# Performance work log

Measured on AMD Instinct MI355X. Metric: run time of the kernel, lower is better.

The kernel has to match this reference:

```python
import jax, jax.numpy as jnp
import numpy as np

N_NODES = 50000


def setup_inputs() -> dict:
    key = jax.random.key(0)
    k1, k2, k3, k4 = jax.random.split(key, 4)
    x = jax.random.normal(k1, (N_NODES, 128), dtype=jnp.float32)
    edge_index = jax.random.randint(k2, (2, 1600000), 0, N_NODES, dtype=jnp.int64)
    W1 = jax.random.normal(k3, (128, 256), dtype=jnp.float32) * (1.0 / np.sqrt(128))
    b1 = jnp.zeros((256,), dtype=jnp.float32)
    W2 = jax.random.normal(k4, (256, 1), dtype=jnp.float32) * (1.0 / np.sqrt(256))
    b2 = jnp.zeros((1,), dtype=jnp.float32)
    return {"x": x, "edge_index": edge_index, "W1": W1, "b1": b1, "W2": W2, "b2": b2}


def _gcn_conv(x, src, dst, norm, W, b, n_nodes):
    # PyG GCNConv: h = X W; out_i = sum_j norm_ij * h_j (+ self loop) + b
    h = x @ W                               # [N, F_out]
    msg = h[src] * norm[:, None]            # [E', F_out] gather + scale
    out = jax.ops.segment_sum(msg, dst, num_segments=n_nodes)  # scatter-add
    return out + b


def reference(x, edge_index, W1, b1, W2, b2):
    n = x.shape[0]
    loop = jnp.arange(n, dtype=edge_index.dtype)
    src = jnp.concatenate([edge_index[0], loop])   # add self loops
    dst = jnp.concatenate([edge_index[1], loop])
    # symmetric degree normalization on A + I
    deg = jax.ops.segment_sum(jnp.ones_like(dst, dtype=x.dtype), dst, num_segments=n)
    dis = jnp.where(deg > 0, jax.lax.rsqrt(deg), 0.0)
    norm = dis[src] * dis[dst]                     # [E']
    h = jax.nn.relu(_gcn_conv(x, src, dst, norm, W1, b1, n))
    return _gcn_conv(h, src, dst, norm, W2, b2, n)
```

## Files before the change

kernel.cpp:

```cpp
#include <hip/hip_runtime.h>


#define EPB_LOG 12
#define EPB (1 << EPB_LOG)
#define BW_LOG 7
#define BW (1 << BW_LOG)
#define MAXBUCK 512
#define SCAN_TILE 2048

typedef __attribute__((ext_vector_type(8))) short bf16x8;
typedef __attribute__((ext_vector_type(4))) float f32x4;

__device__ inline unsigned short f2bf(float f) {
    unsigned int b = __float_as_uint(f);
    unsigned int r = b + 0x7FFFu + ((b >> 16) & 1u);
    return (unsigned short)(r >> 16);
}
__device__ inline float bf_lo(unsigned int u) { return __uint_as_float(u << 16); }
__device__ inline float bf_hi(unsigned int u) { return __uint_as_float(u & 0xFFFF0000u); }

__device__ inline int detect_stride(const int* edges, int t, int* sh) {
    if (t < 64) {
        int v = edges[2 * t + 1];
        unsigned long long bb = __ballot(v != 0);
        if (t == 0) *sh = bb ? 1 : 2;
    }
    __syncthreads();
    return *sh;
}


__global__ __launch_bounds__(256) void k_count(
        const int* __restrict__ edges, const float* __restrict__ W1,
        unsigned short* __restrict__ w1t, int* __restrict__ btot_raw,
        long long E, int nbuck, int nsb) {
    int b = blockIdx.x, t = threadIdx.x;
    if (b >= nsb) {
        int row = (b - nsb) * 2 + (t >> 7);
        int k = t & 127;
        w1t[row * 128 + k] = f2bf(W1[k * 256 + row]);
        return;
    }
    __shared__ int bins[MAXBUCK];
    __shared__ int sh;
    for (int i = t; i < nbuck; i += 256) bins[i] = 0;
    int stride = detect_stride(edges, t, &sh);
    long long base = (long long)b << EPB_LOG;
    long long rem = E - base;
    int nE = (rem < (long long)EPB) ? (int)rem : EPB;
    for (int i = t; i < nE; i += 256) {
        int d = edges[(E + base + i) * stride];
        atomicAdd(&bins[d >> BW_LOG], 1);
    }
    __syncthreads();
    for (int i = t; i < nbuck; i += 256)
        if (bins[i]) atomicAdd(&btot_raw[i], bins[i]);
}

__global__ __launch_bounds__(256) void k_btot_scan(
        const int* __restrict__ btot_raw, int* __restrict__ btot,
        int* __restrict__ curg, int nbuck) {
    __shared__ int ws4[4];
    int t = threadIdx.x;
    int c4 = (nbuck + 255) >> 8;
    int lo = t * c4;
    int hi = lo + c4; if (hi > nbuck) hi = nbuck;
    if (lo > nbuck) lo = nbuck;
    int vals[2];
    int local = 0;
    for (int i = lo; i < hi; ++i) { vals[i - lo] = btot_raw[i]; local += vals[i - lo]; }
    int lane = t & 63, w = t >> 6;
    int inc = local;
    for (int off = 1; off < 64; off <<= 1) {
        int u = __shfl_up(inc, off, 64);
        if (lane >= off) inc += u;
    }
    if (lane == 63) ws4[w] = inc;
    __syncthreads();
    int woff = 0;
    for (int i = 0; i < w; ++i) woff += ws4[i];
    int ex = woff + inc - local;
    for (int i = lo; i < hi; ++i) {
        btot[i] = ex; curg[i] = ex;
        ex += vals[i - lo];
    }
}

__global__ __launch_bounds__(256) void k_partition(
        const int* __restrict__ edges, int* __restrict__ curg,
        unsigned int* __restrict__ part, long long E, int nbuck) {
    __shared__ unsigned int stage[EPB];
    __shared__ unsigned short dst16[EPB];
    __shared__ int bins[MAXBUCK];
    __shared__ int lcur[MAXBUCK];
    __shared__ int gbase[MAXBUCK];
    __shared__ int ws4[4];
    __shared__ int sh;
    int sb = blockIdx.x, t = threadIdx.x;
    for (int i = t; i < nbuck; i += 256) bins[i] = 0;
    int stride = detect_stride(edges, t, &sh);
    long long base = (long long)sb << EPB_LOG;
    long long rem = E - base;
    int nE = (rem < (long long)EPB) ? (int)rem : EPB;
    for (int i = t; i < nE; i += 256) {
        int d = edges[(E + base + i) * stride];
        dst16[i] = (unsigned short)d;
        atomicAdd(&bins[d >> BW_LOG], 1);
    }
    __syncthreads();
    int c4 = (nbuck + 255) >> 8;
    int lo = t * c4;
    int hi = lo + c4; if (hi > nbuck) hi = nbuck;
    if (lo > nbuck) lo = nbuck;
    int vals[2];
    int local = 0;
    for (int i = lo; i < hi; ++i) { vals[i - lo] = bins[i]; local += vals[i - lo]; }
    for (int i = t; i < nbuck; i += 256) {
        int c = bins[i];
        gbase[i] = c ? atomicAdd(&curg[i], c) : 0;
    }
    __syncthreads();
    int lane = t & 63, w = t >> 6;
    int inc = local;
    for (int off = 1; off < 64; off <<= 1) {
        int u = __shfl_up(inc, off, 64);
        if (lane >= off) inc += u;
    }
    if (lane == 63) ws4[w] = inc;
    __syncthreads();
    int woff = 0;
    for (int i = 0; i < w; ++i) woff += ws4[i];
    int ex = woff + inc - local;
    for (int i = lo; i < hi; ++i) {
        bins[i] = ex;
        lcur[i] = ex;
        ex += vals[i - lo];
    }
    __syncthreads();
    for (int i = t; i < nE; i += 256) {
        int s = edges[(base + i) * stride];
        int d = dst16[i];
        int b = d >> BW_LOG;
        int p = atomicAdd(&lcur[b], 1);
        stage[p] = ((unsigned int)s << 16) | (unsigned int)d;
    }
    __syncthreads();
    for (int i = t; i < nE; i += 256) {
        unsigned int pk = stage[i];
        int b = (int)(pk & 0xFFFFu) >> BW_LOG;
        part[gbase[b] + (i - bins[b])] = pk;
    }
}

__global__ __launch_bounds__(256) void k_build_csr(
        const unsigned int* __restrict__ part, const int* __restrict__ btot,
        const float* __restrict__ x, int* __restrict__ row_start,
        float* __restrict__ dis, int* __restrict__ csr_src,
        unsigned short* __restrict__ xs, int nbuck, int n, long long E) {
    __shared__ int c128[BW];
    __shared__ int lcur[BW];
    __shared__ float dld[BW];
    __shared__ int ws2[2];
    int b = blockIdx.x, t = threadIdx.x;
    if (t < BW) c128[t] = 0;
    __syncthreads();
    int start = btot[b];
    int endp = (b + 1 < nbuck) ? btot[b + 1] : (int)E;
    for (int i = start + t; i < endp; i += 256)
        atomicAdd(&c128[part[i] & (BW - 1)], 1);
    __syncthreads();
    int lane = t & 63, w = t >> 6;
    int deg = (t < BW) ? c128[t] : 0;
    int inc = deg;
    for (int off = 1; off < 64; off <<= 1) {
        int u = __shfl_up(inc, off, 64);
        if (lane >= off) inc += u;
    }
    if (t < BW && lane == 63) ws2[w] = inc;
    __syncthreads();
    if (t < BW) {
        int ex = inc - deg + ((w == 1) ? ws2[0] : 0);
        lcur[t] = ex;
        int d = (b << BW_LOG) + t;
        if (d < n) {
            row_start[d] = start + ex;
            float dv = rsqrtf((float)deg + 1.0f);
            dis[d] = dv;
            dld[t] = dv;
        }
    }
    if (b == nbuck - 1 && t == 0) row_start[n] = (int)E;
    __syncthreads();
    for (int i = start + t; i < endp; i += 256) {
        unsigned int pk = part[i];
        int r = atomicAdd(&lcur[pk & (BW - 1)], 1);
        csr_src[start + r] = (int)(pk >> 16);
    }
    int d0 = b << BW_LOG;
    for (int idx = t; idx < BW * 32; idx += 256) {
        int node = d0 + (idx >> 5);
        if (node >= n) break;
        float dv = dld[idx >> 5];
        float4 v = ((const float4*)x)[(size_t)node * 32 + (idx & 31)];
        ushort4 o;
        o.x = f2bf(v.x * dv); o.y = f2bf(v.y * dv);
        o.z = f2bf(v.z * dv); o.w = f2bf(v.w * dv);
        ((ushort4*)xs)[(size_t)node * 32 + (idx & 31)] = o;
    }
}

__global__ __launch_bounds__(256) void k_agg(
        const unsigned short* __restrict__ xs, const int* __restrict__ csr_src,
        const int* __restrict__ row_start, const float* __restrict__ dis,
        unsigned short* __restrict__ aggh, int n) {
    int wid  = (blockIdx.x * blockDim.x + threadIdx.x) >> 6;
    int lane = threadIdx.x & 63;
    if (wid >= n) return;
    int start = row_start[wid], end = row_start[wid + 1];
    const unsigned int* xsu = (const unsigned int*)xs;
    unsigned int self = xsu[((size_t)wid << 6) + lane];
    float acc0 = bf_lo(self);
    float acc1 = bf_hi(self);
    int e = start;
    for (; e + 7 < end; e += 8) {
        int s0 = csr_src[e],     s1 = csr_src[e + 1];
        int s2 = csr_src[e + 2], s3 = csr_src[e + 3];
        int s4 = csr_src[e + 4], s5 = csr_src[e + 5];
        int s6 = csr_src[e + 6], s7 = csr_src[e + 7];
        unsigned int v0 = xsu[((size_t)s0 << 6) + lane];
        unsigned int v1 = xsu[((size_t)s1 << 6) + lane];
        unsigned int v2 = xsu[((size_t)s2 << 6) + lane];
        unsigned int v3 = xsu[((size_t)s3 << 6) + lane];
        unsigned int v4 = xsu[((size_t)s4 << 6) + lane];
        unsigned int v5 = xsu[((size_t)s5 << 6) + lane];
        unsigned int v6 = xsu[((size_t)s6 << 6) + lane];
        unsigned int v7 = xsu[((size_t)s7 << 6) + lane];
        acc0 += bf_lo(v0); acc1 += bf_hi(v0);
        acc0 += bf_lo(v1); acc1 += bf_hi(v1);
        acc0 += bf_lo(v2); acc1 += bf_hi(v2);
        acc0 += bf_lo(v3); acc1 += bf_hi(v3);
        acc0 += bf_lo(v4); acc1 += bf_hi(v4);
        acc0 += bf_lo(v5); acc1 += bf_hi(v5);
        acc0 += bf_lo(v6); acc1 += bf_hi(v6);
        acc0 += bf_lo(v7); acc1 += bf_hi(v7);
    }
    for (; e < end; ++e) {
        int s0 = csr_src[e];
        unsigned int v0 = xsu[((size_t)s0 << 6) + lane];
        acc0 += bf_lo(v0); acc1 += bf_hi(v0);
    }
    float dn = dis[wid];
    unsigned int pack = (unsigned int)f2bf(acc0 * dn) | ((unsigned int)f2bf(acc1 * dn) << 16);
    ((unsigned int*)aggh)[((size_t)wid << 6) + lane] = pack;
}

__global__ __launch_bounds__(256) void k_mm(
        const unsigned short* __restrict__ aggh, const unsigned short* __restrict__ w1t,
        const float* __restrict__ b1, const float* __restrict__ W2,
        const float* __restrict__ dis, float* __restrict__ svs, int n) {
    int wave = threadIdx.x >> 6;
    int lane = threadIdx.x & 63;
    int m    = lane & 15;
    int quad = lane >> 4;
    int node0 = blockIdx.x * 64 + wave * 16;

    bf16x8 afrag[4];
    const unsigned short* arow = aggh + (size_t)(node0 + m) * 128 + quad * 8;
#pragma unroll
    for (int ks = 0; ks < 4; ++ks)
        afrag[ks] = *(const bf16x8*)(arow + ks * 32);

    float p0 = 0.f, p1 = 0.f, p2 = 0.f, p3 = 0.f;
#pragma unroll 1
    for (int tt = 0; tt < 16; ++tt) {
        const unsigned short* brow = w1t + (size_t)(tt * 16 + m) * 128 + quad * 8;
        f32x4 acc = {0.f, 0.f, 0.f, 0.f};
#pragma unroll
        for (int ks = 0; ks < 4; ++ks) {
            bf16x8 bfrag = *(const bf16x8*)(brow + ks * 32);
            acc = __builtin_amdgcn_mfma_f32_16x16x32_bf16(afrag[ks], bfrag, acc, 0, 0, 0);
        }
        int col = tt * 16 + m;
        float bb = b1[col], w2 = W2[col];
        float h0 = acc[0] + bb, h1 = acc[1] + bb, h2 = acc[2] + bb, h3 = acc[3] + bb;
        p0 += (h0 > 0.f ? h0 : 0.f) * w2;
        p1 += (h1 > 0.f ? h1 : 0.f) * w2;
        p2 += (h2 > 0.f ? h2 : 0.f) * w2;
        p3 += (h3 > 0.f ? h3 : 0.f) * w2;
    }
#pragma unroll
    for (int off = 1; off < 16; off <<= 1) {
        p0 += __shfl_xor(p0, off, 64);
        p1 += __shfl_xor(p1, off, 64);
        p2 += __shfl_xor(p2, off, 64);
        p3 += __shfl_xor(p3, off, 64);
    }
    if (m == 0) {
        int nb = node0 + quad * 4;
        if (nb + 0 < n) svs[nb + 0] = p0 * dis[nb + 0];
        if (nb + 1 < n) svs[nb + 1] = p1 * dis[nb + 1];
        if (nb + 2 < n) svs[nb + 2] = p2 * dis[nb + 2];
        if (nb + 3 < n) svs[nb + 3] = p3 * dis[nb + 3];
    }
}

__global__ __launch_bounds__(256) void k_out(
        const float* __restrict__ svs, const int* __restrict__ csr_src,
        const int* __restrict__ row_start, const float* __restrict__ dis,
        const float* __restrict__ b2, float* __restrict__ out, int n) {
    int wid  = (blockIdx.x * blockDim.x + threadIdx.x) >> 6;
    int lane = threadIdx.x & 63;
    if (wid >= n) return;
    int start = row_start[wid], end = row_start[wid + 1];
    float acc = 0.f;
    for (int e = start + lane; e < end; e += 64)
        acc += svs[csr_src[e]];
    for (int off = 32; off; off >>= 1) acc += __shfl_down(acc, off, 64);
    if (lane == 0)
        out[wid] = dis[wid] * (acc + svs[wid]) + b2[0];
}

__global__ void k_init(const int* __restrict__ edges, int* __restrict__ flag,
                       int* __restrict__ cnt, int n) {
    int i = blockIdx.x * blockDim.x + threadIdx.x;
    if (i < n) cnt[i] = 0;
    if (blockIdx.x == 0 && threadIdx.x < 64) {
        int v = edges[2 * threadIdx.x + 1];
        unsigned long long b = __ballot(v != 0);
        if (threadIdx.x == 0) flag[0] = b ? 1 : 2;
    }
}
__global__ __launch_bounds__(128) void k_prep_w(const float* __restrict__ W1,
        unsigned short* __restrict__ w1t) {
    int nn = blockIdx.x, k = threadIdx.x;
    w1t[nn * 128 + k] = f2bf(W1[k * 256 + nn]);
}
__global__ __launch_bounds__(256) void k_prep_xs(const float* __restrict__ x,
        const float* __restrict__ dis, unsigned short* __restrict__ xs, int n) {
    int i = blockIdx.x * 256 + threadIdx.x;
    if (i >= n * 32) return;
    float dsc = dis[i >> 5];
    float4 v = ((const float4*)x)[i];
    ushort4 o;
    o.x = f2bf(v.x * dsc); o.y = f2bf(v.y * dsc);
    o.z = f2bf(v.z * dsc); o.w = f2bf(v.w * dsc);
    ((ushort4*)xs)[i] = o;
}
__global__ void k_count_slow(const int* __restrict__ edges, const int* __restrict__ flag,
                             int* __restrict__ cnt, int* __restrict__ posi, long long E) {
    long long e = (long long)blockIdx.x * blockDim.x + threadIdx.x;
    if (e >= E) return;
    int stride = flag[0];
    int d = edges[(E + e) * stride];
    posi[e] = atomicAdd(&cnt[d], 1);
}
__global__ __launch_bounds__(256) void k_scan_partial(
        const int* __restrict__ cnt, int* __restrict__ bsum, int n) {
    int t = threadIdx.x;
    int idx = blockIdx.x * SCAN_TILE + t * 8;
    int s = 0;
#pragma unroll
    for (int j = 0; j < 8; ++j) { int i = idx + j; if (i < n) s += cnt[i]; }
    for (int off = 32; off; off >>= 1) s += __shfl_down(s, off, 64);
    __shared__ int ws[4];
    if ((t & 63) == 0) ws[t >> 6] = s;
    __syncthreads();
    if (t == 0) bsum[blockIdx.x] = ws[0] + ws[1] + ws[2] + ws[3];
}
__global__ void k_scan_tops(int* __restrict__ bsum, int nb) {
    int t = threadIdx.x;
    int w = (t < nb) ? bsum[t] : 0;
    int v = w;
    for (int off = 1; off < 64; off <<= 1) {
        int u = __shfl_up(v, off, 64);
        if (t >= off) v += u;
    }
    if (t < nb) bsum[t] = v - w;
}
__global__ __launch_bounds__(256) void k_scan_apply(
        const int* __restrict__ cnt, const int* __restrict__ bsum,
        int* __restrict__ row_start, float* __restrict__ dis, int n) {
    int t = threadIdx.x;
    int lane = t & 63, w = t >> 6;
    int idx = blockIdx.x * SCAN_TILE + t * 8;
    int vals[8];
    int s = 0;
#pragma unroll
    for (int j = 0; j < 8; ++j) { int i = idx + j; vals[j] = (i < n) ? cnt[i] : 0; s += vals[j]; }
    int inc = s;
    for (int off = 1; off < 64; off <<= 1) {
        int u = __shfl_up(inc, off, 64);
        if (lane >= off) inc += u;
    }
    __shared__ int wsum[4];
    if (lane == 63) wsum[w] = inc;
    __syncthreads();
    int woff = 0;
    for (int i = 0; i < w; ++i) woff += wsum[i];
    int ex = bsum[blockIdx.x] + woff + inc - s;
#pragma unroll
    for (int j = 0; j < 8; ++j) {
        int i = idx + j;
        if (i < n) {
            row_start[i] = ex;
            dis[i] = rsqrtf((float)vals[j] + 1.0f);
            ex += vals[j];
        }
    }
    if (idx <= n && n < idx + 8) row_start[n] = ex;
}
__global__ void k_scatter_slow(const int* __restrict__ edges, const int* __restrict__ flag,
                               const int* __restrict__ row_start, const int* __restrict__ posi,
                               int* __restrict__ csr_src, long long E) {
    long long e = (long long)blockIdx.x * blockDim.x + threadIdx.x;
    if (e >= E) return;
    int stride = flag[0];
    int s = edges[e * stride];
    int d = edges[(E + e) * stride];
    csr_src[row_start[d] + posi[e]] = s;
}

extern "C" void kernel_launch(void* const* d_in, const int* in_sizes, int n_in,
                              void* d_out, int out_size, void* d_ws, size_t ws_size,
                              hipStream_t stream) {
    const float* x  = (const float*)d_in[0];
    const int*   ei = (const int*)d_in[1];
    const float* W1 = (const float*)d_in[2];
    const float* b1 = (const float*)d_in[3];
    const float* W2 = (const float*)d_in[4];
    const float* b2 = (const float*)d_in[5];
    float* out = (float*)d_out;

    const int N = in_sizes[0] / 128;
    const long long E = in_sizes[1] / 2;
    const int nsb = (int)((E + EPB - 1) >> EPB_LOG);
    const int nbuck = (N + BW - 1) >> BW_LOG;

    char* ws = (char*)d_ws;
    size_t off = 0;
    auto take = [&](size_t bytes) -> char* {
        char* p = ws + off;
        off = (off + bytes + 255) & ~(size_t)255;
        return p;
    };
    int*            flag     = (int*)take(4);
    int*            cnt      = (int*)take((size_t)N * 4);
    int*            rs       = (int*)take((size_t)(N + 1) * 4);
    float*          dis      = (float*)take((size_t)N * 4);
    float*          svs      = (float*)take((size_t)N * 4);
    int*            bsum     = (int*)take(64 * 4);
    int*            btot_raw = (int*)take(MAXBUCK * 4);
    int*            btot     = (int*)take(MAXBUCK * 4);
    int*            curg     = (int*)take(MAXBUCK * 4);
    unsigned int*   part     = (unsigned int*)take((size_t)E * 4);
    int*            csr_src  = (int*)take((size_t)E * 4);
    unsigned short* xs       = (unsigned short*)take((size_t)N * 128 * 2);
    unsigned short* w1t      = (unsigned short*)take((size_t)256 * 128 * 2);
    unsigned short* aggh     = (unsigned short*)take((size_t)(N + 64) * 128 * 2);

    int nb_n  = (N + 255) / 256;
    int nb_e  = (int)((E + 255) / 256);
    int nb_s  = (N + SCAN_TILE - 1) / SCAN_TILE;
    int nb_x  = (N * 32 + 255) / 256;
    int nb_mm = (N + 63) / 64;

    bool fast = (N < 65536);

    if (fast) {
        hipMemsetAsync(btot_raw, 0, (size_t)nbuck * 4, stream);
        k_count    <<<nsb + 128, 256, 0, stream>>>(ei, W1, w1t, btot_raw, E, nbuck, nsb);
        k_btot_scan<<<1, 256, 0, stream>>>(btot_raw, btot, curg, nbuck);
        k_partition<<<nsb, 256, 0, stream>>>(ei, curg, part, E, nbuck);
        k_build_csr<<<nbuck, 256, 0, stream>>>(part, btot, x, rs, dis, csr_src,
                                               xs, nbuck, N, E);
        k_agg      <<<(N + 3) / 4, 256, 0, stream>>>(xs, csr_src, rs, dis, aggh, N);
        k_mm       <<<nb_mm, 256, 0, stream>>>(aggh, w1t, b1, W2, dis, svs, N);
        k_out      <<<(N + 3) / 4, 256, 0, stream>>>(svs, csr_src, rs, dis, b2, out, N);
    } else {
        k_init        <<<nb_n, 256, 0, stream>>>(ei, flag, cnt, N);
        k_prep_w      <<<256, 128, 0, stream>>>(W1, w1t);
        k_count_slow  <<<nb_e, 256, 0, stream>>>(ei, flag, cnt, (int*)part, E);
        k_scan_partial<<<nb_s, 256, 0, stream>>>(cnt, bsum, N);
        k_scan_tops   <<<1, 64, 0, stream>>>(bsum, nb_s);
        k_scan_apply  <<<nb_s, 256, 0, stream>>>(cnt, bsum, rs, dis, N);
        k_prep_xs     <<<nb_x, 256, 0, stream>>>(x, dis, xs, N);
        k_scatter_slow<<<nb_e, 256, 0, stream>>>(ei, flag, rs, (const int*)part, csr_src, E);
        k_agg         <<<(N + 3) / 4, 256, 0, stream>>>(xs, csr_src, rs, dis, aggh, N);
        k_mm          <<<nb_mm, 256, 0, stream>>>(aggh, w1t, b1, W2, dis, svs, N);
        k_out         <<<(N + 3) / 4, 256, 0, stream>>>(svs, csr_src, rs, dis, b2, out, N);
    }
}
```

Before: 242.0 us.

## Split bf16 feature table into column halves for cache-friendly gather aggregation

Stores the scaled bf16 node features as two separate 64-column tables and runs aggregation as two passes, one per half, with each node handled by a half-wave. Each pass gathers from a table half the size, aiming to keep the random neighbour gathers resident in cache. The cost is reading the CSR indices and row offsets twice and using 32-lane groups per node.

```diff
diff --git a/kernel.cpp b/kernel.cpp
--- a/kernel.cpp
+++ b/kernel.cpp
@@ -156,7 +156,8 @@
         const unsigned int* __restrict__ part, const int* __restrict__ btot,
         const float* __restrict__ x, int* __restrict__ row_start,
         float* __restrict__ dis, int* __restrict__ csr_src,
-        unsigned short* __restrict__ xs, int nbuck, int n, long long E) {
+        unsigned short* __restrict__ xs_lo, unsigned short* __restrict__ xs_hi,
+        int nbuck, int n, long long E) {
     __shared__ int c128[BW];
     __shared__ int lcur[BW];
     __shared__ float dld[BW];
@@ -200,58 +201,66 @@
     for (int idx = t; idx < BW * 32; idx += 256) {
         int node = d0 + (idx >> 5);
         if (node >= n) break;
+        int g = idx & 31;
         float dv = dld[idx >> 5];
-        float4 v = ((const float4*)x)[(size_t)node * 32 + (idx & 31)];
+        float4 v = ((const float4*)x)[(size_t)node * 32 + g];
         ushort4 o;
         o.x = f2bf(v.x * dv); o.y = f2bf(v.y * dv);
         o.z = f2bf(v.z * dv); o.w = f2bf(v.w * dv);
-        ((ushort4*)xs)[(size_t)node * 32 + (idx & 31)] = o;
-    }
-}
-
-__global__ __launch_bounds__(256) void k_agg(
-        const unsigned short* __restrict__ xs, const int* __restrict__ csr_src,
-        const int* __restrict__ row_start, const float* __restrict__ dis,
-        unsigned short* __restrict__ aggh, int n) {
-    int wid  = (blockIdx.x * blockDim.x + threadIdx.x) >> 6;
-    int lane = threadIdx.x & 63;
-    if (wid >= n) return;
-    int start = row_start[wid], end = row_start[wid + 1];
-    const unsigned int* xsu = (const unsigned int*)xs;
-    unsigned int self = xsu[((size_t)wid << 6) + lane];
-    float acc0 = bf_lo(self);
-    float acc1 = bf_hi(self);
+        if (g < 16) ((ushort4*)xs_lo)[(size_t)node * 16 + g] = o;
+        else        ((ushort4*)xs_hi)[(size_t)node * 16 + (g - 16)] = o;
+    }
+}
+
+__global__ __launch_bounds__(256) void k_agg_split(
+        const unsigned short* __restrict__ xs_lo,
+        const unsigned short* __restrict__ xs_hi,
+        const int* __restrict__ csr_src, const int* __restrict__ rs,
+        const float* __restrict__ dis, unsigned short* __restrict__ aggh,
+        int n, int NBH) {
+    int half = (blockIdx.x < NBH) ? 0 : 1;
+    int bi   = (half == 0) ? blockIdx.x : blockIdx.x - NBH;
+    int t = threadIdx.x;
+    int lane = t & 63, w = t >> 6;
+    int hw = lane >> 5;
+    int hl = lane & 31;
+    int node = bi * 8 + w * 2 + hw;
+    if (node >= n) return;
+    const unsigned int* xsu = (const unsigned int*)(half ? xs_hi : xs_lo);
+    int start = rs[node], end = rs[node + 1];
+    unsigned int self = xsu[((size_t)node << 5) + hl];
+    float a0 = bf_lo(self), a1 = bf_hi(self);
     int e = start;
     for (; e + 7 < end; e += 8) {
         int s0 = csr_src[e],     s1 = csr_src[e + 1];
         int s2 = csr_src[e + 2], s3 = csr_src[e + 3];
         int s4 = csr_src[e + 4], s5 = csr_src[e + 5];
         int s6 = csr_src[e + 6], s7 = csr_src[e + 7];
-        unsigned int v0 = xsu[((size_t)s0 << 6) + lane];
-        unsigned int v1 = xsu[((size_t)s1 << 6) + lane];
-        unsigned int v2 = xsu[((size_t)s2 << 6) + lane];
-        unsigned int v3 = xsu[((size_t)s3 << 6) + lane];
-        unsigned int v4 = xsu[((size_t)s4 << 6) + lane];
-        unsigned int v5 = xsu[((size_t)s5 << 6) + lane];
-        unsigned int v6 = xsu[((size_t)s6 << 6) + lane];
-        unsigned int v7 = xsu[((size_t)s7 << 6) + lane];
-        acc0 += bf_lo(v0); acc1 += bf_hi(v0);
-        acc0 += bf_lo(v1); acc1 += bf_hi(v1);
-        acc0 += bf_lo(v2); acc1 += bf_hi(v2);
-        acc0 += bf_lo(v3); acc1 += bf_hi(v3);
-        acc0 += bf_lo(v4); acc1 += bf_hi(v4);
-        acc0 += bf_lo(v5); acc1 += bf_hi(v5);
-        acc0 += bf_lo(v6); acc1 += bf_hi(v6);
-        acc0 += bf_lo(v7); acc1 += bf_hi(v7);
+        unsigned int v0 = xsu[((size_t)s0 << 5) + hl];
+        unsigned int v1 = xsu[((size_t)s1 << 5) + hl];
+        unsigned int v2 = xsu[((size_t)s2 << 5) + hl];
+        unsigned int v3 = xsu[((size_t)s3 << 5) + hl];
+        unsigned int v4 = xsu[((size_t)s4 << 5) + hl];
+        unsigned int v5 = xsu[((size_t)s5 << 5) + hl];
+        unsigned int v6 = xsu[((size_t)s6 << 5) + hl];
+        unsigned int v7 = xsu[((size_t)s7 << 5) + hl];
+        a0 += bf_lo(v0); a1 += bf_hi(v0);
+        a0 += bf_lo(v1); a1 += bf_hi(v1);
+        a0 += bf_lo(v2); a1 += bf_hi(v2);
+        a0 += bf_lo(v3); a1 += bf_hi(v3);
+        a0 += bf_lo(v4); a1 += bf_hi(v4);
+        a0 += bf_lo(v5); a1 += bf_hi(v5);
+        a0 += bf_lo(v6); a1 += bf_hi(v6);
+        a0 += bf_lo(v7); a1 += bf_hi(v7);
     }
     for (; e < end; ++e) {
         int s0 = csr_src[e];
-        unsigned int v0 = xsu[((size_t)s0 << 6) + lane];
-        acc0 += bf_lo(v0); acc1 += bf_hi(v0);
-    }
-    float dn = dis[wid];
-    unsigned int pack = (unsigned int)f2bf(acc0 * dn) | ((unsigned int)f2bf(acc1 * dn) << 16);
-    ((unsigned int*)aggh)[((size_t)wid << 6) + lane] = pack;
+        unsigned int v0 = xsu[((size_t)s0 << 5) + hl];
+        a0 += bf_lo(v0); a1 += bf_hi(v0);
+    }
+    float dn = dis[node];
+    unsigned int pack = (unsigned int)f2bf(a0 * dn) | ((unsigned int)f2bf(a1 * dn) << 16);
+    ((unsigned int*)aggh)[((size_t)node << 6) + (half << 5) + hl] = pack;
 }
 
 __global__ __launch_bounds__(256) void k_mm(
@@ -330,21 +339,24 @@
         if (threadIdx.x == 0) flag[0] = b ? 1 : 2;
     }
 }
+__global__ __launch_bounds__(256) void k_prep_xs(const float* __restrict__ x,
+        const float* __restrict__ dis, unsigned short* __restrict__ xs_lo,
+        unsigned short* __restrict__ xs_hi, int n) {
+    int i = blockIdx.x * 256 + threadIdx.x;
+    if (i >= n * 32) return;
+    int node = i >> 5, g = i & 31;
+    float dsc = dis[node];
+    float4 v = ((const float4*)x)[i];
+    ushort4 o;
+    o.x = f2bf(v.x * dsc); o.y = f2bf(v.y * dsc);
+    o.z = f2bf(v.z * dsc); o.w = f2bf(v.w * dsc);
+    if (g < 16) ((ushort4*)xs_lo)[(size_t)node * 16 + g] = o;
+    else        ((ushort4*)xs_hi)[(size_t)node * 16 + (g - 16)] = o;
+}
 __global__ __launch_bounds__(128) void k_prep_w(const float* __restrict__ W1,
         unsigned short* __restrict__ w1t) {
     int nn = blockIdx.x, k = threadIdx.x;
     w1t[nn * 128 + k] = f2bf(W1[k * 256 + nn]);
-}
-__global__ __launch_bounds__(256) void k_prep_xs(const float* __restrict__ x,
-        const float* __restrict__ dis, unsigned short* __restrict__ xs, int n) {
-    int i = blockIdx.x * 256 + threadIdx.x;
-    if (i >= n * 32) return;
-    float dsc = dis[i >> 5];
-    float4 v = ((const float4*)x)[i];
-    ushort4 o;
-    o.x = f2bf(v.x * dsc); o.y = f2bf(v.y * dsc);
-    o.z = f2bf(v.z * dsc); o.w = f2bf(v.w * dsc);
-    ((ushort4*)xs)[i] = o;
 }
 __global__ void k_count_slow(const int* __restrict__ edges, const int* __restrict__ flag,
                              int* __restrict__ cnt, int* __restrict__ posi, long long E) {
@@ -454,7 +466,8 @@
     int*            curg     = (int*)take(MAXBUCK * 4);
     unsigned int*   part     = (unsigned int*)take((size_t)E * 4);
     int*            csr_src  = (int*)take((size_t)E * 4);
-    unsigned short* xs       = (unsigned short*)take((size_t)N * 128 * 2);
+    unsigned short* xs_lo    = (unsigned short*)take((size_t)N * 64 * 2);
+    unsigned short* xs_hi    = (unsigned short*)take((size_t)N * 64 * 2);
     unsigned short* w1t      = (unsigned short*)take((size_t)256 * 128 * 2);
     unsigned short* aggh     = (unsigned short*)take((size_t)(N + 64) * 128 * 2);
 
@@ -462,7 +475,7 @@
     int nb_e  = (int)((E + 255) / 256);
     int nb_s  = (N + SCAN_TILE - 1) / SCAN_TILE;
     int nb_x  = (N * 32 + 255) / 256;
-    int nb_mm = (N + 63) / 64;
+    int NBH   = (N + 7) / 8;
 
     bool fast = (N < 65536);
 
@@ -472,9 +485,10 @@
         k_btot_scan<<<1, 256, 0, stream>>>(btot_raw, btot, curg, nbuck);
         k_partition<<<nsb, 256, 0, stream>>>(ei, curg, part, E, nbuck);
         k_build_csr<<<nbuck, 256, 0, stream>>>(part, btot, x, rs, dis, csr_src,
-                                               xs, nbuck, N, E);
-        k_agg      <<<(N + 3) / 4, 256, 0, stream>>>(xs, csr_src, rs, dis, aggh, N);
-        k_mm       <<<nb_mm, 256, 0, stream>>>(aggh, w1t, b1, W2, dis, svs, N);
+                                               xs_lo, xs_hi, nbuck, N, E);
+        k_agg_split<<<2 * NBH, 256, 0, stream>>>(xs_lo, xs_hi, csr_src, rs, dis,
+                                                 aggh, N, NBH);
+        k_mm       <<<(N + 63) / 64, 256, 0, stream>>>(aggh, w1t, b1, W2, dis, svs, N);
         k_out      <<<(N + 3) / 4, 256, 0, stream>>>(svs, csr_src, rs, dis, b2, out, N);
     } else {
         k_init        <<<nb_n, 256, 0, stream>>>(ei, flag, cnt, N);
@@ -483,10 +497,11 @@
         k_scan_partial<<<nb_s, 256, 0, stream>>>(cnt, bsum, N);
         k_scan_tops   <<<1, 64, 0, stream>>>(bsum, nb_s);
         k_scan_apply  <<<nb_s, 256, 0, stream>>>(cnt, bsum, rs, dis, N);
-        k_prep_xs     <<<nb_x, 256, 0, stream>>>(x, dis, xs, N);
+        k_prep_xs     <<<nb_x, 256, 0, stream>>>(x, dis, xs_lo, xs_hi, N);
         k_scatter_slow<<<nb_e, 256, 0, stream>>>(ei, flag, rs, (const int*)part, csr_src, E);
-        k_agg         <<<(N + 3) / 4, 256, 0, stream>>>(xs, csr_src, rs, dis, aggh, N);
-        k_mm          <<<nb_mm, 256, 0, stream>>>(aggh, w1t, b1, W2, dis, svs, N);
+        k_agg_split   <<<2 * NBH, 256, 0, stream>>>(xs_lo, xs_hi, csr_src, rs, dis,
+                                                    aggh, N, NBH);
+        k_mm          <<<(N + 63) / 64, 256, 0, stream>>>(aggh, w1t, b1, W2, dis, svs, N);
         k_out         <<<(N + 3) / 4, 256, 0, stream>>>(svs, csr_src, rs, dis, b2, out, N);
     }
 }
```

New measurement: 240.7 us. No clear change (-0.5%).
